# Kernel optimization log

Hardware: AMD Instinct MI355X
Metric: run time of the kernel (lower is better)

## Reference

```python
import jax, jax.numpy as jnp
import numpy as np

HEAD_SIZE = 64

def setup_inputs() -> dict:
    key = jax.random.key(0)
    k1, k2, k3, k4 = jax.random.split(key, 4)
    B, T, C = 4, 4096, 1024
    x = jax.random.normal(k1, (B, T, C), dtype=jnp.float32)
    Wk = jax.random.normal(k2, (C, HEAD_SIZE), dtype=jnp.float32) * (C ** -0.5)
    Wq = jax.random.normal(k3, (C, HEAD_SIZE), dtype=jnp.float32) * (C ** -0.5)
    Wv = jax.random.normal(k4, (C, HEAD_SIZE), dtype=jnp.float32) * (C ** -0.5)
    return {"x": x, "Wk": Wk, "Wq": Wq, "Wv": Wv}

def reference(x, Wk, Wq, Wv):
    # x: [B, T, C]; projections to [B, T, H]
    T = x.shape[1]
    k = jnp.einsum('btc,ch->bth', x, Wk)
    q = jnp.einsum('btc,ch->bth', x, Wq)
    v = jnp.einsum('btc,ch->bth', x, Wv)
    scale = jnp.asarray(HEAD_SIZE ** -0.5, dtype=x.dtype)
    scores = jnp.einsum('bqh,bkh->bqk', q, k) * scale  # [B, T, T]
    causal = jnp.tril(jnp.ones((T, T), dtype=bool))
    scores = jnp.where(causal, scores, jnp.asarray(-jnp.inf, dtype=scores.dtype))
    attn = jax.nn.softmax(scores, axis=-1)  # dropout is identity in eval mode
    out = jnp.einsum('bqk,bkh->bqh', attn, v)
    return out
```

## Files before the change

### kernel.cpp

```cpp
#include <hip/hip_runtime.h>
#include <hip/hip_bf16.h>
#include <math.h>

#define NB 4
#define NT 4096
#define NC 1024
#define NH 64
#define NCH 144

typedef __attribute__((ext_vector_type(8))) short short8;
typedef __attribute__((ext_vector_type(4))) float f32x4;
typedef __attribute__((ext_vector_type(8))) unsigned short ushort8v;
typedef __attribute__((ext_vector_type(4))) unsigned short ushort4v;

static __device__ __forceinline__ unsigned short f2bf(float f) {
    union { __hip_bfloat16 b; unsigned short u; } cv;
    cv.b = __float2bfloat16(f);
    return cv.u;
}
static __device__ __forceinline__ float bf2f(unsigned short u) {
    union { unsigned int i; float f; } cv;
    cv.i = ((unsigned int)u) << 16;
    return cv.f;
}

__global__ __launch_bounds__(256) void wprep_kernel(
    const float* __restrict__ Wk,
    const float* __restrict__ Wq,
    const float* __restrict__ Wv,
    unsigned short* __restrict__ wt)
{
    __shared__ float tile[64][65];
    const int m  = blockIdx.x >> 4;
    const int k0 = (blockIdx.x & 15) << 6;
    const float* __restrict__ W = (m == 0) ? Wk : (m == 1) ? Wq : Wv;
    const float qs = (m == 1) ? 0.125f * 1.44269504f : 1.0f;
    const int tid = threadIdx.x;
    const int c   = tid & 63;
    for (int i = tid >> 6; i < 64; i += 4)
        tile[i][c] = W[(size_t)(k0 + i) * NH + c];
    __syncthreads();
    const int i0 = (tid >> 6) * 16;
    unsigned short* dst = wt + ((size_t)m * 64 + c) * NC + k0 + i0;
    ushort8v a, b;
#pragma unroll
    for (int j = 0; j < 8; ++j) a[j] = f2bf(tile[i0 + j][c] * qs);
#pragma unroll
    for (int j = 0; j < 8; ++j) b[j] = f2bf(tile[i0 + 8 + j][c] * qs);
    *reinterpret_cast<ushort8v*>(dst)     = a;
    *reinterpret_cast<ushort8v*>(dst + 8) = b;
}

__global__ __launch_bounds__(256, 2) void proj_kernel(
    const float* __restrict__ x,
    const unsigned short* __restrict__ wt,
    unsigned short* __restrict__ ko,
    unsigned short* __restrict__ qo,
    unsigned short* __restrict__ vt)
{
    __shared__ unsigned short xsb[2][32 * 64];
    __shared__ unsigned short wsb[2][192 * 64];

    const int tid  = threadIdx.x;
    const int wid  = tid >> 6;
    const int lane = tid & 63;
    const int l15  = lane & 15;
    const int hi   = lane >> 4;
    const int t0   = blockIdx.x << 5;

    const int srow = tid >> 3;
    const int sg   = tid & 7;
    const int ssw  = sg ^ (srow & 7);
    const float* __restrict__ xsrc = x + (size_t)(t0 + srow) * NC + sg * 8;
    unsigned short* const sdst0 = &xsb[0][srow * 64 + ssw * 8];
    unsigned short* const sdst1 = &xsb[1][srow * 64 + ssw * 8];

    int wrow[6], wsl[6];
#pragma unroll
    for (int it = 0; it < 6; ++it) {
        const int F = it * 256 + tid;
        wrow[it] = F >> 3;
        wsl[it]  = F & 7;
    }

    int mm[3], hr[3];
#pragma unroll
    for (int f = 0; f < 3; ++f) {
        const int hc = wid * 48 + f * 16;
        mm[f] = hc >> 6;
        hr[f] = hc & 63;
    }

    f32x4 acc[2][3];
#pragma unroll
    for (int mf = 0; mf < 2; ++mf)
#pragma unroll
        for (int f = 0; f < 3; ++f) acc[mf][f] = (f32x4){0.f, 0.f, 0.f, 0.f};

    auto XWRITE = [&](unsigned short* dst, const f32x4& a, const f32x4& b) {
        ushort8v pk;
        pk[0] = f2bf(a[0]); pk[1] = f2bf(a[1]);
        pk[2] = f2bf(a[2]); pk[3] = f2bf(a[3]);
        pk[4] = f2bf(b[0]); pk[5] = f2bf(b[1]);
        pk[6] = f2bf(b[2]); pk[7] = f2bf(b[3]);
        *reinterpret_cast<ushort8v*>(dst) = pk;
    };

    auto WSTORE = [&](int bi, const short8 (&wr)[6]) {
#pragma unroll
        for (int it = 0; it < 6; ++it) {
            const int dst = wrow[it] * 64 + ((wsl[it] ^ (wrow[it] & 7)) << 3);
            *reinterpret_cast<short8*>(&wsb[bi][dst]) = wr[it];
        }
    };

    auto COMPUTE = [&](int bi) {
        short8 xf[2][2];
#pragma unroll
        for (int mf = 0; mf < 2; ++mf) {
            const int row = mf * 16 + l15;
#pragma unroll
            for (int ks = 0; ks < 2; ++ks) {
                const int sw = (ks * 4 + hi) ^ (row & 7);
                xf[mf][ks] = *reinterpret_cast<const short8*>(
                    &xsb[bi][row * 64 + sw * 8]);
            }
        }
#pragma unroll
        for (int f = 0; f < 3; ++f) {
            const int wr = wid * 48 + f * 16 + l15;
            const int r7 = l15 & 7;
#pragma unroll
            for (int ks = 0; ks < 2; ++ks) {
                const short8 wf = *reinterpret_cast<const short8*>(
                    &wsb[bi][wr * 64 + (((hi + ks * 4) ^ r7) << 3)]);
                if (mm[f] == 2) {
#pragma unroll
                    for (int mf = 0; mf < 2; ++mf)
                        acc[mf][f] = __builtin_amdgcn_mfma_f32_16x16x32_bf16(
                            xf[mf][ks], wf, acc[mf][f], 0, 0, 0);
                } else {
#pragma unroll
                    for (int mf = 0; mf < 2; ++mf)
                        acc[mf][f] = __builtin_amdgcn_mfma_f32_16x16x32_bf16(
                            wf, xf[mf][ks], acc[mf][f], 0, 0, 0);
                }
            }
        }
    };

    {
        const f32x4 a = *reinterpret_cast<const f32x4*>(xsrc);
        const f32x4 b = *reinterpret_cast<const f32x4*>(xsrc + 4);
        XWRITE(sdst0, a, b);
        short8 wr[6];
#pragma unroll
        for (int it = 0; it < 6; ++it)
            wr[it] = *reinterpret_cast<const short8*>(
                wt + (size_t)wrow[it] * NC + wsl[it] * 8);
        WSTORE(0, wr);
    }
    __syncthreads();

    for (int ck = 0; ck < 16; ++ck) {
        const int cur = ck & 1;
        f32x4 na, nb;
        short8 wr[6];
        if (ck < 15) {
            const float* p = xsrc + (ck + 1) * 64;
            na = *reinterpret_cast<const f32x4*>(p);
            nb = *reinterpret_cast<const f32x4*>(p + 4);
#pragma unroll
            for (int it = 0; it < 6; ++it)
                wr[it] = *reinterpret_cast<const short8*>(
                    wt + (size_t)wrow[it] * NC + (ck + 1) * 64 + wsl[it] * 8);
        }
        COMPUTE(cur);
        if (ck < 15) {
            XWRITE(cur ? sdst0 : sdst1, na, nb);
            WSTORE(cur ^ 1, wr);
        }
        __syncthreads();
    }

    const int b  = t0 >> 12;
    const int tl = t0 & (NT - 1);
#pragma unroll
    for (int f = 0; f < 3; ++f) {
#pragma unroll
        for (int mf = 0; mf < 2; ++mf) {
            const f32x4 a = acc[mf][f];
            ushort4v pk;
            pk[0] = f2bf(a[0]); pk[1] = f2bf(a[1]);
            pk[2] = f2bf(a[2]); pk[3] = f2bf(a[3]);
            if (mm[f] == 2) {
                unsigned short* d = vt + ((size_t)(b * NH + hr[f] + l15)) * NT
                                       + tl + mf * 16 + hi * 4;
                *reinterpret_cast<ushort4v*>(d) = pk;
            } else {
                unsigned short* o = (mm[f] == 0) ? ko : qo;
                unsigned short* d = o + (size_t)(t0 + mf * 16 + l15) * NH
                                      + hr[f] + hi * 4;
                *reinterpret_cast<ushort4v*>(d) = pk;
            }
        }
    }
}

__global__ __launch_bounds__(512) void attn_kernel(
    const unsigned short* __restrict__ kin,
    const unsigned short* __restrict__ qin,
    const unsigned short* __restrict__ vt,
    unsigned short* __restrict__ part)
{
    __shared__ unsigned short ksb[2][64 * 64];
    __shared__ unsigned short vsb[2][64 * 64];
    __shared__ unsigned short p_lds[8][16 * 72];

    const int tid  = threadIdx.x;
    const int wid  = tid >> 6;
    const int lane = tid & 63;
    const int q15  = lane & 15;
    const int hi   = lane >> 4;

    const int bid  = blockIdx.x;
    const int xcd  = bid & 7;
    const int b    = xcd >> 1;
    const int clin = ((bid >> 3) << 1) | (xcd & 1);
    const int c    = (NCH - 1) - clin;

    int qi = 0, basei = 0;
    for (int t = 31; t >= 0; --t) {
        const int g = t >> 2, r = t & 3;
        const int bs = t + 2 * g * (g - 1) + r * g;
        if (bs <= c) { qi = t; basei = bs; break; }
    }
    const int k     = c - basei;
    const int n_blk = 2 * qi + 2;
    const int jb0   = k * 8;
    const int jend  = min(jb0 + 8, n_blk);
    const int n_w   = 2 * qi + 1 + (wid >> 2);

    const unsigned short* kb = kin + (size_t)b * NT * NH;
    const unsigned short* qb = qin + (size_t)b * NT * NH;
    const unsigned short* vb = vt  + (size_t)b * NH * NT;

    const int gq = qi * 128 + wid * 16 + q15;

    short8 qf0, qf1;
    {
        const unsigned short* qrow = qb + (size_t)gq * NH + hi * 8;
        qf0 = *reinterpret_cast<const short8*>(qrow);
        qf1 = *reinterpret_cast<const short8*>(qrow + 32);
    }

    const int srow = tid >> 3;
    const int sg   = tid & 7;
    const int sdst = srow * 64 + (sg ^ (srow & 7)) * 8;
    const unsigned short* kstat = kb + (size_t)srow * NH + sg * 8;
    const unsigned short* vstat = vb + (size_t)srow * NT + sg * 8;

    f32x4 ot[4];
#pragma unroll
    for (int i = 0; i < 4; ++i) ot[i] = (f32x4){0.f, 0.f, 0.f, 0.f};
    float m = 0.f, lp = 0.f;

    {
        const short8 kr = *reinterpret_cast<const short8*>(kstat + (size_t)jb0 * 4096);
        const short8 vr = *reinterpret_cast<const short8*>(vstat + jb0 * 64);
        *reinterpret_cast<short8*>(&ksb[0][sdst]) = kr;
        *reinterpret_cast<short8*>(&vsb[0][sdst]) = vr;
    }
    __syncthreads();

    int cur = 0;
    for (int jb = jb0; jb < jend; ++jb) {
        const bool more = (jb + 1 < jend);
        short8 knx, vnx;
        if (more) {
            knx = *reinterpret_cast<const short8*>(kstat + (size_t)(jb + 1) * 4096);
            vnx = *reinterpret_cast<const short8*>(vstat + (jb + 1) * 64);
        }

        if (jb < n_w) {
            const int kv0 = jb << 6;
            const int r7  = q15 & 7;

            f32x4 st[4];
            __builtin_amdgcn_s_setprio(1);
#pragma unroll
            for (int kt = 0; kt < 4; ++kt) {
                const int rb = (kt * 16 + q15) * 64;
                const short8 ka0 = *reinterpret_cast<const short8*>(
                    &ksb[cur][rb + ((hi ^ r7) * 8)]);
                const short8 ka1 = *reinterpret_cast<const short8*>(
                    &ksb[cur][rb + (((4 + hi) ^ r7) * 8)]);
                f32x4 acc = (f32x4){0.f, 0.f, 0.f, 0.f};
                acc = __builtin_amdgcn_mfma_f32_16x16x32_bf16(ka0, qf0, acc, 0, 0, 0);
                acc = __builtin_amdgcn_mfma_f32_16x16x32_bf16(ka1, qf1, acc, 0, 0, 0);
                st[kt] = acc;
            }
            __builtin_amdgcn_s_setprio(0);

            float tmax4 = -INFINITY;
            if (jb == n_w - 1) {
#pragma unroll
                for (int kt = 0; kt < 4; ++kt)
#pragma unroll
                    for (int r = 0; r < 4; ++r) {
                        const int gk = kv0 + kt * 16 + hi * 4 + r;
                        const float s = (gk <= gq) ? st[kt][r] : -INFINITY;
                        st[kt][r] = s;
                        tmax4 = fmaxf(tmax4, s);
                    }
            } else {
#pragma unroll
                for (int kt = 0; kt < 4; ++kt)
#pragma unroll
                    for (int r = 0; r < 4; ++r)
                        tmax4 = fmaxf(tmax4, st[kt][r]);
            }

            if (!__all(tmax4 <= m + 11.5f)) {
                float tm = fmaxf(tmax4, __shfl_xor(tmax4, 16));
                tm = fmaxf(tm, __shfl_xor(tm, 32));
                const float mnew = fmaxf(m, tm);
                const float corr = __builtin_amdgcn_exp2f(m - mnew);
                lp *= corr;
#pragma unroll
                for (int i = 0; i < 4; ++i) {
                    ot[i][0] *= corr; ot[i][1] *= corr;
                    ot[i][2] *= corr; ot[i][3] *= corr;
                }
                m = mnew;
            }

#pragma unroll
            for (int kt = 0; kt < 4; ++kt) {
                const float p0 = __builtin_amdgcn_exp2f(st[kt][0] - m);
                const float p1 = __builtin_amdgcn_exp2f(st[kt][1] - m);
                const float p2 = __builtin_amdgcn_exp2f(st[kt][2] - m);
                const float p3 = __builtin_amdgcn_exp2f(st[kt][3] - m);
                lp += (p0 + p1) + (p2 + p3);
                ushort4v pk;
                pk[0] = f2bf(p0); pk[1] = f2bf(p1);
                pk[2] = f2bf(p2); pk[3] = f2bf(p3);
                *reinterpret_cast<ushort4v*>(&p_lds[wid][q15 * 72 + kt * 16 + hi * 4]) = pk;
            }

            const short8 pb0 = *reinterpret_cast<const short8*>(&p_lds[wid][q15 * 72 + hi * 8]);
            const short8 pb1 = *reinterpret_cast<const short8*>(&p_lds[wid][q15 * 72 + 32 + hi * 8]);
            __builtin_amdgcn_s_setprio(1);
#pragma unroll
            for (int ht = 0; ht < 4; ++ht) {
                const int rb = (ht * 16 + q15) * 64;
                const short8 va0 = *reinterpret_cast<const short8*>(
                    &vsb[cur][rb + ((hi ^ r7) * 8)]);
                const short8 va1 = *reinterpret_cast<const short8*>(
                    &vsb[cur][rb + (((4 + hi) ^ r7) * 8)]);
                ot[ht] = __builtin_amdgcn_mfma_f32_16x16x32_bf16(va0, pb0, ot[ht], 0, 0, 0);
                ot[ht] = __builtin_amdgcn_mfma_f32_16x16x32_bf16(va1, pb1, ot[ht], 0, 0, 0);
            }
            __builtin_amdgcn_s_setprio(0);
        }

        if (more) {
            *reinterpret_cast<short8*>(&ksb[cur ^ 1][sdst]) = knx;
            *reinterpret_cast<short8*>(&vsb[cur ^ 1][sdst]) = vnx;
        }
        __syncthreads();
        cur ^= 1;
    }

    float l = lp + __shfl_xor(lp, 16);
    l += __shfl_xor(l, 32);
    unsigned short* pp = part + (((size_t)b * NCH + c) * 128 + wid * 16 + q15) * 72;
#pragma unroll
    for (int ht = 0; ht < 4; ++ht) {
        ushort4v pk;
        pk[0] = f2bf(ot[ht][0]); pk[1] = f2bf(ot[ht][1]);
        pk[2] = f2bf(ot[ht][2]); pk[3] = f2bf(ot[ht][3]);
        *reinterpret_cast<ushort4v*>(pp + ht * 16 + hi * 4) = pk;
    }
    if (hi == 0) {
        *reinterpret_cast<float*>(pp + 64) = m;
        *reinterpret_cast<float*>(pp + 66) = l;
    }
}

__global__ __launch_bounds__(256) void comb_kernel(
    const unsigned short* __restrict__ part,
    float* __restrict__ outp)
{
    const int tid = threadIdx.x;
    const int bid = blockIdx.x;
    const int b   = bid >> 10;
    const int lr  = ((bid & 1023) << 2) + (tid >> 6);
    const int h   = tid & 63;
    const int qi  = lr >> 7;
    const int g   = qi >> 2, r = qi & 3;
    const int basei = qi + 2 * g * (g - 1) + r * g;
    const int nch   = (qi >> 2) + 1;
    const unsigned short* p0 = part + (((size_t)b * NCH + basei) * 128 + (lr & 127)) * 72;

    float mg = -INFINITY;
    for (int ch = 0; ch < nch; ++ch)
        mg = fmaxf(mg, *reinterpret_cast<const float*>(p0 + (size_t)ch * 128 * 72 + 64));
    float L = 0.f, o = 0.f;
    for (int ch = 0; ch < nch; ++ch) {
        const unsigned short* pc = p0 + (size_t)ch * 128 * 72;
        const float mc = *reinterpret_cast<const float*>(pc + 64);
        const float lc = *reinterpret_cast<const float*>(pc + 66);
        const float w  = __builtin_amdgcn_exp2f(mc - mg);
        L += w * lc;
        o += w * bf2f(pc[h]);
    }
    outp[((size_t)b * NT + lr) * NH + h] = o / L;
}

extern "C" void kernel_launch(void* const* d_in, const int* in_sizes, int n_in,
                              void* d_out, int out_size, void* d_ws, size_t ws_size,
                              hipStream_t stream) {
    const float* x  = (const float*)d_in[0];
    const float* Wk = (const float*)d_in[1];
    const float* Wq = (const float*)d_in[2];
    const float* Wv = (const float*)d_in[3];
    float* out = (float*)d_out;

    unsigned short* kbuf = (unsigned short*)d_ws;
    unsigned short* qbuf = kbuf + (size_t)NB * NT * NH;
    unsigned short* vtbf = qbuf + (size_t)NB * NT * NH;
    unsigned short* wtbf = vtbf + (size_t)NB * NT * NH;
    unsigned short* part = wtbf + (size_t)3 * 64 * NC;

    wprep_kernel<<<48, 256, 0, stream>>>(Wk, Wq, Wv, wtbf);
    proj_kernel<<<NB * NT / 32, 256, 0, stream>>>(x, wtbf, kbuf, qbuf, vtbf);
    attn_kernel<<<576, 512, 0, stream>>>(kbuf, qbuf, vtbf, part);
    comb_kernel<<<4096, 256, 0, stream>>>(part, out);
}
```

Measured before the change: 61.77 us.

## Single-buffer projection LDS tiles to raise occupancy in proj_kernel

Replaces the double-buffered x and W shared-memory tiles in the projection kernel with single buffers. A second barrier per chunk now guards the buffer before it is overwritten, and launch bounds are raised to target 4 blocks per CU instead of 2. The goal is to halve LDS use so more blocks fit per CU and hide latency. The cost is an extra __syncthreads per iteration, less intra-block overlap of stores with compute, and tighter register limits.

```diff
diff --git a/kernel.cpp b/kernel.cpp
--- a/kernel.cpp
+++ b/kernel.cpp
@@ -51,15 +51,15 @@
     *reinterpret_cast<ushort8v*>(dst + 8) = b;
 }
 
-__global__ __launch_bounds__(256, 2) void proj_kernel(
+__global__ __launch_bounds__(256, 4) void proj_kernel(
     const float* __restrict__ x,
     const unsigned short* __restrict__ wt,
     unsigned short* __restrict__ ko,
     unsigned short* __restrict__ qo,
     unsigned short* __restrict__ vt)
 {
-    __shared__ unsigned short xsb[2][32 * 64];
-    __shared__ unsigned short wsb[2][192 * 64];
+    __shared__ unsigned short xsb[32 * 64];
+    __shared__ unsigned short wsb[192 * 64];
 
     const int tid  = threadIdx.x;
     const int wid  = tid >> 6;
@@ -72,8 +72,7 @@
     const int sg   = tid & 7;
     const int ssw  = sg ^ (srow & 7);
     const float* __restrict__ xsrc = x + (size_t)(t0 + srow) * NC + sg * 8;
-    unsigned short* const sdst0 = &xsb[0][srow * 64 + ssw * 8];
-    unsigned short* const sdst1 = &xsb[1][srow * 64 + ssw * 8];
+    unsigned short* const sdst = &xsb[srow * 64 + ssw * 8];
 
     int wrow[6], wsl[6];
 #pragma unroll
@@ -97,24 +96,24 @@
 #pragma unroll
         for (int f = 0; f < 3; ++f) acc[mf][f] = (f32x4){0.f, 0.f, 0.f, 0.f};
 
-    auto XWRITE = [&](unsigned short* dst, const f32x4& a, const f32x4& b) {
+    auto XWRITE = [&](const f32x4& a, const f32x4& b) {
         ushort8v pk;
         pk[0] = f2bf(a[0]); pk[1] = f2bf(a[1]);
         pk[2] = f2bf(a[2]); pk[3] = f2bf(a[3]);
         pk[4] = f2bf(b[0]); pk[5] = f2bf(b[1]);
         pk[6] = f2bf(b[2]); pk[7] = f2bf(b[3]);
-        *reinterpret_cast<ushort8v*>(dst) = pk;
+        *reinterpret_cast<ushort8v*>(sdst) = pk;
     };
 
-    auto WSTORE = [&](int bi, const short8 (&wr)[6]) {
+    auto WSTORE = [&](const short8 (&wr)[6]) {
 #pragma unroll
         for (int it = 0; it < 6; ++it) {
             const int dst = wrow[it] * 64 + ((wsl[it] ^ (wrow[it] & 7)) << 3);
-            *reinterpret_cast<short8*>(&wsb[bi][dst]) = wr[it];
+            *reinterpret_cast<short8*>(&wsb[dst]) = wr[it];
         }
     };
 
-    auto COMPUTE = [&](int bi) {
+    auto COMPUTE = [&]() {
         short8 xf[2][2];
 #pragma unroll
         for (int mf = 0; mf < 2; ++mf) {
@@ -123,7 +122,7 @@
             for (int ks = 0; ks < 2; ++ks) {
                 const int sw = (ks * 4 + hi) ^ (row & 7);
                 xf[mf][ks] = *reinterpret_cast<const short8*>(
-                    &xsb[bi][row * 64 + sw * 8]);
+                    &xsb[row * 64 + sw * 8]);
             }
         }
 #pragma unroll
@@ -133,7 +132,7 @@
 #pragma unroll
             for (int ks = 0; ks < 2; ++ks) {
                 const short8 wf = *reinterpret_cast<const short8*>(
-                    &wsb[bi][wr * 64 + (((hi + ks * 4) ^ r7) << 3)]);
+                    &wsb[wr * 64 + (((hi + ks * 4) ^ r7) << 3)]);
                 if (mm[f] == 2) {
 #pragma unroll
                     for (int mf = 0; mf < 2; ++mf)
@@ -152,18 +151,17 @@
     {
         const f32x4 a = *reinterpret_cast<const f32x4*>(xsrc);
         const f32x4 b = *reinterpret_cast<const f32x4*>(xsrc + 4);
-        XWRITE(sdst0, a, b);
+        XWRITE(a, b);
         short8 wr[6];
 #pragma unroll
         for (int it = 0; it < 6; ++it)
             wr[it] = *reinterpret_cast<const short8*>(
                 wt + (size_t)wrow[it] * NC + wsl[it] * 8);
-        WSTORE(0, wr);
+        WSTORE(wr);
     }
     __syncthreads();
 
     for (int ck = 0; ck < 16; ++ck) {
-        const int cur = ck & 1;
         f32x4 na, nb;
         short8 wr[6];
         if (ck < 15) {
@@ -175,12 +173,13 @@
                 wr[it] = *reinterpret_cast<const short8*>(
                     wt + (size_t)wrow[it] * NC + (ck + 1) * 64 + wsl[it] * 8);
         }
-        COMPUTE(cur);
+        COMPUTE();
         if (ck < 15) {
-            XWRITE(cur ? sdst0 : sdst1, na, nb);
-            WSTORE(cur ^ 1, wr);
-        }
-        __syncthreads();
+            __syncthreads();
+            XWRITE(na, nb);
+            WSTORE(wr);
+            __syncthreads();
+        }
     }
 
     const int b  = t0 >> 12;
```

Result: no change. 62.02 us (+0.4%).
